# Kernel tuning notes

Measured on AMD Instinct MI355X. Metric: run time of the kernel, lower is better.

The kernel has to match this reference:

```python
import jax, jax.numpy as jnp
import numpy as np

HEADS = 8
DIM_HEAD = 64
SCALE = DIM_HEAD ** -0.5


def setup_inputs() -> dict:
    key = jax.random.key(0)
    k1, k2, k3 = jax.random.split(key, 3)
    B, N, D = 4, 2048, 512
    inner = HEADS * DIM_HEAD  # 512
    x = jax.random.normal(k1, (B, N, D), dtype=jnp.float32)
    # nn.Linear stores weight [out, in]; y = x @ W.T
    w_qkv = jax.random.normal(k2, (3 * inner, D), dtype=jnp.float32) * (D ** -0.5)
    w_out = jax.random.normal(k3, (D, inner), dtype=jnp.float32) * (inner ** -0.5)
    b_out = jnp.zeros((D,), dtype=jnp.float32)
    return {"x": x, "w_qkv": w_qkv, "w_out": w_out, "b_out": b_out}


def reference(x, w_qkv, w_out, b_out):
    B, N, D = x.shape
    qkv = jnp.einsum('bnd,ed->bne', x, w_qkv)  # [B,N,3*inner]
    q, k, v = jnp.split(qkv, 3, axis=-1)
    def to_heads(t):
        return t.reshape(B, N, HEADS, DIM_HEAD).transpose(0, 2, 1, 3)  # [B,H,N,Dh]
    q, k, v = to_heads(q), to_heads(k), to_heads(v)
    dots = jnp.einsum('bhid,bhjd->bhij', q, k) * SCALE  # [B,H,N,N]
    attn = jax.nn.softmax(dots, axis=-1)
    out = jnp.einsum('bhij,bhjd->bhid', attn, v)  # [B,H,N,Dh]
    out = out.transpose(0, 2, 1, 3).reshape(B, N, HEADS * DIM_HEAD)
    return jnp.einsum('bne,de->bnd', out, w_out) + b_out
```

## Files before the change

kernel.cpp:

```cpp
#include <hip/hip_runtime.h>
#include <hip/hip_bf16.h>
#include <stdint.h>

typedef __bf16 bf16;
typedef __bf16 bf16x8 __attribute__((ext_vector_type(8)));
typedef __bf16 bf16x4 __attribute__((ext_vector_type(4)));
typedef float f32x4 __attribute__((ext_vector_type(4)));

template <int V> struct Int { static constexpr int value = V; };

static __device__ __forceinline__ void gl2lds16(const void* g, void* l) {
  const __attribute__((address_space(1))) void* gp =
      reinterpret_cast<const __attribute__((address_space(1))) void*>(
          reinterpret_cast<uintptr_t>(g));
  __attribute__((address_space(3))) void* lp =
      reinterpret_cast<__attribute__((address_space(3))) void*>(
          static_cast<uint32_t>(reinterpret_cast<uintptr_t>(l)));
  __builtin_amdgcn_global_load_lds(gp, lp, 16, 0, 0);
}

static __device__ __forceinline__ float fast_exp2(float x) {
#if __has_builtin(__builtin_amdgcn_exp2f)
  return __builtin_amdgcn_exp2f(x);
#else
  return exp2f(x);
#endif
}

__global__ __launch_bounds__(256) void cvt_all(const float* __restrict__ x,
                                               const float* __restrict__ wq,
                                               const float* __restrict__ wo,
                                               bf16* __restrict__ dst) {
  int i = blockIdx.x * 256 + threadIdx.x;
  const int stride = gridDim.x * 256;
  for (; i < 1310720; i += stride) {
    const float4 v = (i < 1048576) ? reinterpret_cast<const float4*>(x)[i]
                   : (i < 1245184) ? reinterpret_cast<const float4*>(wq)[i - 1048576]
                                   : reinterpret_cast<const float4*>(wo)[i - 1245184];
    bf16x4 o;
    o[0] = (bf16)v.x; o[1] = (bf16)v.y; o[2] = (bf16)v.z; o[3] = (bf16)v.w;
    reinterpret_cast<bf16x4*>(dst)[i] = o;
  }
}

__global__ __launch_bounds__(256) void qkv_gemm(const bf16* __restrict__ X,
                                                const bf16* __restrict__ W,
                                                bf16* __restrict__ Qb,
                                                bf16* __restrict__ Kb,
                                                bf16* __restrict__ Vt) {
  __shared__ __align__(16) bf16 AshX[8192];
  __shared__ __align__(16) bf16 BshX[8192];
  const int t = threadIdx.x;
  const int lane = t & 63;
  const int w = t >> 6;
  const int fr = lane & 15, fg = lane >> 4;
  const int wr = w >> 1, wc = w & 1;
  const int m0 = blockIdx.x * 128;
  const int n0 = blockIdx.y * 128;
  const int r0 = t >> 2, seg = t & 3;
  const bf16* pA0 = X + (m0 + r0) * 512 + seg * 8;
  const bf16* pA1 = X + (m0 + r0 + 64) * 512 + seg * 8;
  const bf16* pB0 = W + (n0 + r0) * 512 + seg * 8;
  const bf16* pB1 = W + (n0 + r0 + 64) * 512 + seg * 8;
  const bf16* ap = AshX + (wr * 64 + fr) * 32 + fg * 8;
  const bf16* bp = BshX + (wc * 64 + fr) * 32 + fg * 8;

  f32x4 acc[4][4] = {};

  auto stage = [&](auto Bt) {
    constexpr int B = decltype(Bt)::value;
    gl2lds16(pA0, (void*)(AshX + B * 4096 + t * 8));
    gl2lds16(pA1, (void*)(AshX + B * 4096 + 2048 + t * 8));
    gl2lds16(pB0, (void*)(BshX + B * 4096 + t * 8));
    gl2lds16(pB1, (void*)(BshX + B * 4096 + 2048 + t * 8));
    pA0 += 32; pA1 += 32; pB0 += 32; pB1 += 32;
  };
  auto step = [&](auto Bt) {
    constexpr int B = decltype(Bt)::value;
    bf16x8 a[4], b[4];
#pragma unroll
    for (int m = 0; m < 4; ++m) a[m] = *reinterpret_cast<const bf16x8*>(ap + B * 4096 + m * 512);
#pragma unroll
    for (int n = 0; n < 4; ++n) b[n] = *reinterpret_cast<const bf16x8*>(bp + B * 4096 + n * 512);
#pragma unroll
    for (int m = 0; m < 4; ++m)
#pragma unroll
      for (int n = 0; n < 4; ++n)
        acc[m][n] = __builtin_amdgcn_mfma_f32_16x16x32_bf16(a[m], b[n], acc[m][n], 0, 0, 0);
  };

  stage(Int<0>{});
  __syncthreads();
  for (int kt = 0; kt < 16; kt += 2) {
    stage(Int<1>{});
    step(Int<0>{});
    __syncthreads();
    if (kt < 14) stage(Int<0>{});
    step(Int<1>{});
    __syncthreads();
  }

  const int which = n0 >> 9;
#pragma unroll
  for (int n = 0; n < 4; ++n) {
    const int e = n0 + wc * 64 + 16 * n + fr;
    const int h = (e >> 6) & 7;
    const int d = e & 63;
#pragma unroll
    for (int m = 0; m < 4; ++m) {
      const int mbase = m0 + wr * 64 + 16 * m + fg * 4;
      if (which == 2) {
        bf16x4 pk;
#pragma unroll
        for (int r = 0; r < 4; ++r) pk[r] = (bf16)acc[m][n][r];
        const int b = mbase >> 11, tok = mbase & 2047;
        *reinterpret_cast<bf16x4*>(&Vt[((b * 8 + h) * 64 + d) * 2048 + tok]) = pk;
      } else {
        bf16* dst = (which == 0) ? Qb : Kb;
        const float sc = (which == 0) ? (0.125f * 1.44269504088896f) : 1.0f;
#pragma unroll
        for (int r = 0; r < 4; ++r) {
          const int row = mbase + r;
          const int b = row >> 11, tok = row & 2047;
          dst[((b * 8 + h) * 2048 + tok) * 64 + d] = (bf16)(acc[m][n][r] * sc);
        }
      }
    }
  }
}

__global__ __launch_bounds__(256, 4) void attn_fwd(const bf16* __restrict__ Qb,
                                                   const bf16* __restrict__ Kb,
                                                   const bf16* __restrict__ Vt,
                                                   bf16* __restrict__ Ob) {
  __shared__ __align__(16) bf16 sh[16384];
  const int t = threadIdx.x;
  const int lane = t & 63;
  const int w = t >> 6;
  const int fr = lane & 15, fg = lane >> 4;
  const int bh = blockIdx.x;
  const int q0 = blockIdx.y * 64 + 16 * w;

  const bf16* Qrow = Qb + (bh * 2048 + q0 + fr) * 64;
  const bf16x8 qf0 = *reinterpret_cast<const bf16x8*>(Qrow + fg * 8);
  const bf16x8 qf1 = *reinterpret_cast<const bf16x8*>(Qrow + 32 + fg * 8);

  bf16x8 ones;
#pragma unroll
  for (int i = 0; i < 8; ++i) ones[i] = (bf16)1.0f;

  const int c0row = t >> 3, cseg = t & 7;
  const int c1row = c0row + 32;
  const int s0 = (cseg ^ (c0row & 7)) * 8;
  const int s1 = (cseg ^ (c1row & 7)) * 8;
  const int kp0 = 32 * ((c0row >> 4) >> 1) + 8 * ((c0row & 15) >> 2) +
                  4 * ((c0row >> 4) & 1) + (c0row & 3);
  const int kp1 = 32 * ((c1row >> 4) >> 1) + 8 * ((c1row & 15) >> 2) +
                  4 * ((c1row >> 4) & 1) + (c1row & 3);
  const bf16* pK0 = Kb + bh * 131072 + kp0 * 64 + s0;
  const bf16* pK1 = Kb + bh * 131072 + kp1 * 64 + s1;
  const bf16* pV0 = Vt + bh * 131072 + c0row * 2048 + s0;
  const bf16* pV1 = Vt + bh * 131072 + c1row * 2048 + s1;

  const int swz = (fr & 7) << 4;
  const int ko0 = fr * 128 + ((fg * 16) ^ swz);
  const int ko1 = fr * 128 + ((64 + fg * 16) ^ swz);
  const char* shb = reinterpret_cast<const char*>(sh);

  f32x4 oacc[4] = {};
  f32x4 lacc = {};
  const f32x4 fzero = {0.f, 0.f, 0.f, 0.f};

  auto stage = [&](auto St) {
    constexpr int S = decltype(St)::value;
    gl2lds16(pK0, (void*)(sh + S * 4096 + t * 8));
    gl2lds16(pK1, (void*)(sh + S * 4096 + 2048 + t * 8));
    gl2lds16(pV0, (void*)(sh + 8192 + S * 4096 + t * 8));
    gl2lds16(pV1, (void*)(sh + 8192 + S * 4096 + 2048 + t * 8));
    pK0 += 4096; pK1 += 4096; pV0 += 64; pV1 += 64;
  };

  auto compute = [&](auto St) {
    constexpr int S = decltype(St)::value;
    f32x4 s[4];
#pragma unroll
    for (int j = 0; j < 4; ++j) {
      const bf16x8 kf0 = *reinterpret_cast<const bf16x8*>(shb + ko0 + (S * 8192 + j * 2048));
      s[j] = __builtin_amdgcn_mfma_f32_16x16x32_bf16(kf0, qf0, fzero, 0, 0, 0);
      const bf16x8 kf1 = *reinterpret_cast<const bf16x8*>(shb + ko1 + (S * 8192 + j * 2048));
      s[j] = __builtin_amdgcn_mfma_f32_16x16x32_bf16(kf1, qf1, s[j], 0, 0, 0);
    }
    bf16x8 pf0;
#pragma unroll
    for (int j = 0; j < 2; ++j)
#pragma unroll
      for (int r = 0; r < 4; ++r) pf0[4 * j + r] = (bf16)fast_exp2(s[j][r]);
    __builtin_amdgcn_s_setprio(1);
    lacc = __builtin_amdgcn_mfma_f32_16x16x32_bf16(ones, pf0, lacc, 0, 0, 0);
#pragma unroll
    for (int j = 0; j < 4; ++j) {
      const bf16x8 vf = *reinterpret_cast<const bf16x8*>(
          shb + ko0 + (16384 + S * 8192 + j * 2048));
      oacc[j] = __builtin_amdgcn_mfma_f32_16x16x32_bf16(vf, pf0, oacc[j], 0, 0, 0);
    }
    __builtin_amdgcn_s_setprio(0);
    bf16x8 pf1;
#pragma unroll
    for (int j = 2; j < 4; ++j)
#pragma unroll
      for (int r = 0; r < 4; ++r) pf1[4 * (j - 2) + r] = (bf16)fast_exp2(s[j][r]);
    __builtin_amdgcn_s_setprio(1);
    lacc = __builtin_amdgcn_mfma_f32_16x16x32_bf16(ones, pf1, lacc, 0, 0, 0);
#pragma unroll
    for (int j = 0; j < 4; ++j) {
      const bf16x8 vf = *reinterpret_cast<const bf16x8*>(
          shb + ko1 + (16384 + S * 8192 + j * 2048));
      oacc[j] = __builtin_amdgcn_mfma_f32_16x16x32_bf16(vf, pf1, oacc[j], 0, 0, 0);
    }
    __builtin_amdgcn_s_setprio(0);
  };

  stage(Int<0>{});
  __syncthreads();
  for (int kt = 0; kt < 32; kt += 2) {
    stage(Int<1>{});
    compute(Int<0>{});
    __syncthreads();
    if (kt < 30) stage(Int<0>{});
    compute(Int<1>{});
    __syncthreads();
  }

  const int b = bh >> 3, h = bh & 7;
  const int q = q0 + fr;
  const float inv = 1.0f / lacc[0];
#pragma unroll
  for (int j = 0; j < 4; ++j) {
    bf16x4 o4;
#pragma unroll
    for (int r = 0; r < 4; ++r) o4[r] = (bf16)(oacc[j][r] * inv);
    *reinterpret_cast<bf16x4*>(&Ob[(b * 2048 + q) * 512 + h * 64 + 16 * j + 4 * fg]) = o4;
  }
}

__global__ __launch_bounds__(256) void out_gemm(const bf16* __restrict__ O,
                                                const bf16* __restrict__ W,
                                                const float* __restrict__ bias,
                                                float* __restrict__ Y) {
  __shared__ __align__(16) bf16 Ash[2][64 * 32];
  __shared__ __align__(16) bf16 Bsh[2][64 * 32];
  const int t = threadIdx.x;
  const int lane = t & 63;
  const int w = t >> 6;
  const int fr = lane & 15, fg = lane >> 4;
  const int m0 = blockIdx.x * 64;
  const int n0 = blockIdx.y * 64;
  const int srow = t >> 2, sseg = t & 3;
  const bf16* gA = O + (m0 + srow) * 512 + sseg * 8;
  const bf16* gB = W + (n0 + srow) * 512 + sseg * 8;

  f32x4 acc[4] = {};
  gl2lds16(gA, &Ash[0][t * 8]);
  gl2lds16(gB, &Bsh[0][t * 8]);
  __syncthreads();
  int cur = 0;
  for (int kt = 0; kt < 16; ++kt) {
    if (kt < 15) {
      gl2lds16(gA + (kt + 1) * 32, &Ash[cur ^ 1][t * 8]);
      gl2lds16(gB + (kt + 1) * 32, &Bsh[cur ^ 1][t * 8]);
    }
    const bf16x8 a = *reinterpret_cast<const bf16x8*>(&Ash[cur][(16 * w + fr) * 32 + fg * 8]);
#pragma unroll
    for (int j = 0; j < 4; ++j) {
      const bf16x8 b = *reinterpret_cast<const bf16x8*>(&Bsh[cur][(16 * j + fr) * 32 + fg * 8]);
      acc[j] = __builtin_amdgcn_mfma_f32_16x16x32_bf16(a, b, acc[j], 0, 0, 0);
    }
    __syncthreads();
    cur ^= 1;
  }
  const int mbase = m0 + 16 * w + fg * 4;
#pragma unroll
  for (int j = 0; j < 4; ++j) {
    const int col = n0 + 16 * j + fr;
    const float bv = bias[col];
#pragma unroll
    for (int r = 0; r < 4; ++r) {
      Y[(mbase + r) * 512 + col] = acc[j][r] + bv;
    }
  }
}

extern "C" void kernel_launch(void* const* d_in, const int* in_sizes, int n_in,
                              void* d_out, int out_size, void* d_ws, size_t ws_size,
                              hipStream_t stream) {
  const float* x = (const float*)d_in[0];
  const float* w_qkv = (const float*)d_in[1];
  const float* w_out = (const float*)d_in[2];
  const float* b_out = (const float*)d_in[3];
  float* y = (float*)d_out;
  char* ws = (char*)d_ws;
  bf16* xb    = (bf16*)(ws);
  bf16* wqkvb = (bf16*)(ws + 8388608);
  bf16* woutb = (bf16*)(ws + 9961472);
  bf16* Qb    = (bf16*)(ws + 10485760);
  bf16* Kb    = (bf16*)(ws + 18874368);
  bf16* Vt    = (bf16*)(ws + 27262976);
  bf16* Ob    = (bf16*)(ws + 35651584);

  hipLaunchKernelGGL(cvt_all, dim3(5120), dim3(256), 0, stream, x, w_qkv, w_out, xb);
  hipLaunchKernelGGL(qkv_gemm, dim3(64, 12), dim3(256), 0, stream, xb, wqkvb, Qb, Kb, Vt);
  hipLaunchKernelGGL(attn_fwd, dim3(32, 32), dim3(256), 0, stream, Qb, Kb, Vt, Ob);
  hipLaunchKernelGGL(out_gemm, dim3(128, 8), dim3(256), 0, stream, Ob, woutb, b_out, y);
}
```

Before: 83.75 us.

## Process two 16-row query tiles per wave to reuse K/V LDS fragments

```diff
diff --git a/kernel.cpp b/kernel.cpp
--- a/kernel.cpp
+++ b/kernel.cpp
@@ -129,7 +129,7 @@
   }
 }
 
-__global__ __launch_bounds__(256, 4) void attn_fwd(const bf16* __restrict__ Qb,
+__global__ __launch_bounds__(256, 2) void attn_fwd(const bf16* __restrict__ Qb,
                                                    const bf16* __restrict__ Kb,
                                                    const bf16* __restrict__ Vt,
                                                    bf16* __restrict__ Ob) {
@@ -139,11 +139,13 @@
   const int w = t >> 6;
   const int fr = lane & 15, fg = lane >> 4;
   const int bh = blockIdx.x;
-  const int q0 = blockIdx.y * 64 + 16 * w;
+  const int q0 = blockIdx.y * 128 + 32 * w;
 
   const bf16* Qrow = Qb + (bh * 2048 + q0 + fr) * 64;
-  const bf16x8 qf0 = *reinterpret_cast<const bf16x8*>(Qrow + fg * 8);
-  const bf16x8 qf1 = *reinterpret_cast<const bf16x8*>(Qrow + 32 + fg * 8);
+  const bf16x8 qa0 = *reinterpret_cast<const bf16x8*>(Qrow + fg * 8);
+  const bf16x8 qa1 = *reinterpret_cast<const bf16x8*>(Qrow + 32 + fg * 8);
+  const bf16x8 qb0 = *reinterpret_cast<const bf16x8*>(Qrow + 1024 + fg * 8);
+  const bf16x8 qb1 = *reinterpret_cast<const bf16x8*>(Qrow + 1024 + 32 + fg * 8);
 
   bf16x8 ones;
 #pragma unroll
@@ -167,8 +169,8 @@
   const int ko1 = fr * 128 + ((64 + fg * 16) ^ swz);
   const char* shb = reinterpret_cast<const char*>(sh);
 
-  f32x4 oacc[4] = {};
-  f32x4 lacc = {};
+  f32x4 oA[4] = {}, oB[4] = {};
+  f32x4 lA = {}, lB = {};
   const f32x4 fzero = {0.f, 0.f, 0.f, 0.f};
 
   auto stage = [&](auto St) {
@@ -182,40 +184,52 @@
 
   auto compute = [&](auto St) {
     constexpr int S = decltype(St)::value;
-    f32x4 s[4];
+    f32x4 sA[4], sB[4];
 #pragma unroll
     for (int j = 0; j < 4; ++j) {
       const bf16x8 kf0 = *reinterpret_cast<const bf16x8*>(shb + ko0 + (S * 8192 + j * 2048));
-      s[j] = __builtin_amdgcn_mfma_f32_16x16x32_bf16(kf0, qf0, fzero, 0, 0, 0);
+      sA[j] = __builtin_amdgcn_mfma_f32_16x16x32_bf16(kf0, qa0, fzero, 0, 0, 0);
+      sB[j] = __builtin_amdgcn_mfma_f32_16x16x32_bf16(kf0, qb0, fzero, 0, 0, 0);
       const bf16x8 kf1 = *reinterpret_cast<const bf16x8*>(shb + ko1 + (S * 8192 + j * 2048));
-      s[j] = __builtin_amdgcn_mfma_f32_16x16x32_bf16(kf1, qf1, s[j], 0, 0, 0);
-    }
-    bf16x8 pf0;
+      sA[j] = __builtin_amdgcn_mfma_f32_16x16x32_bf16(kf1, qa1, sA[j], 0, 0, 0);
+      sB[j] = __builtin_amdgcn_mfma_f32_16x16x32_bf16(kf1, qb1, sB[j], 0, 0, 0);
+    }
+    bf16x8 pA0, pB0;
 #pragma unroll
     for (int j = 0; j < 2; ++j)
 #pragma unroll
-      for (int r = 0; r < 4; ++r) pf0[4 * j + r] = (bf16)fast_exp2(s[j][r]);
+      for (int r = 0; r < 4; ++r) {
+        pA0[4 * j + r] = (bf16)fast_exp2(sA[j][r]);
+        pB0[4 * j + r] = (bf16)fast_exp2(sB[j][r]);
+      }
     __builtin_amdgcn_s_setprio(1);
-    lacc = __builtin_amdgcn_mfma_f32_16x16x32_bf16(ones, pf0, lacc, 0, 0, 0);
+    lA = __builtin_amdgcn_mfma_f32_16x16x32_bf16(ones, pA0, lA, 0, 0, 0);
+    lB = __builtin_amdgcn_mfma_f32_16x16x32_bf16(ones, pB0, lB, 0, 0, 0);
 #pragma unroll
     for (int j = 0; j < 4; ++j) {
       const bf16x8 vf = *reinterpret_cast<const bf16x8*>(
           shb + ko0 + (16384 + S * 8192 + j * 2048));
-      oacc[j] = __builtin_amdgcn_mfma_f32_16x16x32_bf16(vf, pf0, oacc[j], 0, 0, 0);
+      oA[j] = __builtin_amdgcn_mfma_f32_16x16x32_bf16(vf, pA0, oA[j], 0, 0, 0);
+      oB[j] = __builtin_amdgcn_mfma_f32_16x16x32_bf16(vf, pB0, oB[j], 0, 0, 0);
     }
     __builtin_amdgcn_s_setprio(0);
-    bf16x8 pf1;
+    bf16x8 pA1, pB1;
 #pragma unroll
     for (int j = 2; j < 4; ++j)
 #pragma unroll
-      for (int r = 0; r < 4; ++r) pf1[4 * (j - 2) + r] = (bf16)fast_exp2(s[j][r]);
+      for (int r = 0; r < 4; ++r) {
+        pA1[4 * (j - 2) + r] = (bf16)fast_exp2(sA[j][r]);
+        pB1[4 * (j - 2) + r] = (bf16)fast_exp2(sB[j][r]);
+      }
     __builtin_amdgcn_s_setprio(1);
-    lacc = __builtin_amdgcn_mfma_f32_16x16x32_bf16(ones, pf1, lacc, 0, 0, 0);
+    lA = __builtin_amdgcn_mfma_f32_16x16x32_bf16(ones, pA1, lA, 0, 0, 0);
+    lB = __builtin_amdgcn_mfma_f32_16x16x32_bf16(ones, pB1, lB, 0, 0, 0);
 #pragma unroll
     for (int j = 0; j < 4; ++j) {
       const bf16x8 vf = *reinterpret_cast<const bf16x8*>(
           shb + ko1 + (16384 + S * 8192 + j * 2048));
-      oacc[j] = __builtin_amdgcn_mfma_f32_16x16x32_bf16(vf, pf1, oacc[j], 0, 0, 0);
+      oA[j] = __builtin_amdgcn_mfma_f32_16x16x32_bf16(vf, pA1, oA[j], 0, 0, 0);
+      oB[j] = __builtin_amdgcn_mfma_f32_16x16x32_bf16(vf, pB1, oB[j], 0, 0, 0);
     }
     __builtin_amdgcn_s_setprio(0);
   };
@@ -232,14 +246,18 @@
   }
 
   const int b = bh >> 3, h = bh & 7;
-  const int q = q0 + fr;
-  const float inv = 1.0f / lacc[0];
+  const int qA = q0 + fr;
+  const float invA = 1.0f / lA[0];
+  const float invB = 1.0f / lB[0];
 #pragma unroll
   for (int j = 0; j < 4; ++j) {
     bf16x4 o4;
 #pragma unroll
-    for (int r = 0; r < 4; ++r) o4[r] = (bf16)(oacc[j][r] * inv);
-    *reinterpret_cast<bf16x4*>(&Ob[(b * 2048 + q) * 512 + h * 64 + 16 * j + 4 * fg]) = o4;
+    for (int r = 0; r < 4; ++r) o4[r] = (bf16)(oA[j][r] * invA);
+    *reinterpret_cast<bf16x4*>(&Ob[(b * 2048 + qA) * 512 + h * 64 + 16 * j + 4 * fg]) = o4;
+#pragma unroll
+    for (int r = 0; r < 4; ++r) o4[r] = (bf16)(oB[j][r] * invB);
+    *reinterpret_cast<bf16x4*>(&Ob[(b * 2048 + qA + 16) * 512 + h * 64 + 16 * j + 4 * fg]) = o4;
   }
 }
 
@@ -309,6 +327,6 @@
 
   hipLaunchKernelGGL(cvt_all, dim3(5120), dim3(256), 0, stream, x, w_qkv, w_out, xb);
   hipLaunchKernelGGL(qkv_gemm, dim3(64, 12), dim3(256), 0, stream, xb, wqkvb, Qb, Kb, Vt);
-  hipLaunchKernelGGL(attn_fwd, dim3(32, 32), dim3(256), 0, stream, Qb, Kb, Vt, Ob);
+  hipLaunchKernelGGL(attn_fwd, dim3(32, 16), dim3(256), 0, stream, Qb, Kb, Vt, Ob);
   hipLaunchKernelGGL(out_gemm, dim3(128, 8), dim3(256), 0, stream, Ob, woutb, b_out, y);
 }
```

Measured after the change: 76.94 us (median of 2 runs). 1.09x faster.
